# Kernel tuning notes

Hardware: AMD Instinct MI355X
Metric: run time of the kernel (lower is better)

## Reference

```python
import jax, jax.numpy as jnp
import numpy as np

N, E, G = 32768, 262144, 1024
FIN, ED = 32, 8
H, C = 4, 64            # gat_heads, graph_hidden_dim
HC = H * C              # 256
FP_IN, DESC_IN = 2048, 200
GOUT, FPOUT, DOUT = 64, 256, 64
TIN = GOUT + FPOUT + DOUT  # 384
NT = 12
BN_EPS = 1e-5


def bn_eval(x, gamma, beta):
    # eval-mode BatchNorm1d with default running stats (mean=0, var=1)
    inv = 1.0 / jnp.sqrt(1.0 + BN_EPS)
    return x * (gamma * inv) + beta


def gatv2(x, edge_index, edge_attr, Wl, bl, Wr, br, We, att, bias):
    """PyG GATv2Conv (concat heads, add_self_loops=True, fill_value='mean')."""
    n = x.shape[0]
    src, dst = edge_index[0], edge_index[1]
    # self-loop edge_attr = mean of incoming edge_attr per node (PyG fill_value='mean')
    deg = jax.ops.segment_sum(jnp.ones(src.shape, x.dtype), dst, n)
    ea_loop = jax.ops.segment_sum(edge_attr, dst, n) / jnp.maximum(deg, 1.0)[:, None]
    loop = jnp.arange(n)
    src = jnp.concatenate([src, loop])
    dst = jnp.concatenate([dst, loop])
    ea = jnp.concatenate([edge_attr, ea_loop], axis=0)
    xl = (x @ Wl + bl).reshape(n, H, C)   # source transform
    xr = (x @ Wr + br).reshape(n, H, C)   # target transform
    ee = (ea @ We).reshape(-1, H, C)      # edge transform (no bias in PyG)
    m = jax.nn.leaky_relu(xl[src] + xr[dst] + ee, 0.2)  # [E', H, C]
    logit = jnp.einsum('ehc,hc->eh', m, att)            # [E', H]
    # segment softmax over incoming edges of each target node
    lmax = jax.ops.segment_max(logit, dst, n)
    p = jnp.exp(logit - lmax[dst])
    alpha = p / jax.ops.segment_sum(p, dst, n)[dst]
    out = jax.ops.segment_sum(xl[src] * alpha[:, :, None], dst, n)  # [n, H, C]
    return out.reshape(n, HC) + bias


def setup_inputs() -> dict:
    key = jax.random.key(0)
    ks = iter(jax.random.split(key, 64))

    def p(shape, scale=0.05):
        return jax.random.normal(next(ks), shape, dtype=jnp.float32) * scale

    inp = {}
    inp['x'] = jax.random.normal(next(ks), (N, FIN), dtype=jnp.float32)
    inp['edge_index'] = jax.random.randint(next(ks), (2, E), 0, N, dtype=jnp.int32)
    inp['edge_attr'] = jax.random.normal(next(ks), (E, ED), dtype=jnp.float32)
    inp['batch'] = (jnp.arange(N) * G) // N          # sorted, covers all G graphs
    inp['fp'] = jax.random.uniform(next(ks), (G, FP_IN), dtype=jnp.float32)
    inp['desc'] = jax.random.normal(next(ks), (G, DESC_IN), dtype=jnp.float32)
    # GATv2 layer 1 (in=FIN) and layer 2 (in=HC)
    for tag, fin in (('c1', FIN), ('c2', HC)):
        inp[tag + '_Wl'] = p((fin, HC))
        inp[tag + '_bl'] = p((HC,))
        inp[tag + '_Wr'] = p((fin, HC))
        inp[tag + '_br'] = p((HC,))
        inp[tag + '_We'] = p((ED, HC))
        inp[tag + '_att'] = p((H, C))
        inp[tag + '_bias'] = p((HC,))
    inp['gW'], inp['gb'] = p((HC, GOUT)), p((GOUT,))
    inp['g_gn'], inp['g_bt'] = jnp.ones((GOUT,)), jnp.zeros((GOUT,))
    inp['fW'], inp['fb'] = p((FP_IN, FPOUT)), p((FPOUT,))
    inp['f_gn'], inp['f_bt'] = jnp.ones((FPOUT,)), jnp.zeros((FPOUT,))
    inp['dW'], inp['db'] = p((DESC_IN, DOUT)), p((DOUT,))
    inp['d_gn'], inp['d_bt'] = jnp.ones((DOUT,)), jnp.zeros((DOUT,))
    inp['k1W'], inp['k1b'] = p((TIN, TIN // 2)), p((TIN // 2,))
    inp['k1_gn'], inp['k1_bt'] = jnp.ones((TIN // 2,)), jnp.zeros((TIN // 2,))
    inp['k2W'], inp['k2b'] = p((TIN // 2, TIN // 4)), p((TIN // 4,))
    inp['k2_gn'], inp['k2_bt'] = jnp.ones((TIN // 4,)), jnp.zeros((TIN // 4,))
    inp['k3W'], inp['k3b'] = p((TIN // 4, NT)), p((NT,))
    return inp


def reference(x, edge_index, edge_attr, batch, fp, desc,
              c1_Wl, c1_bl, c1_Wr, c1_br, c1_We, c1_att, c1_bias,
              c2_Wl, c2_bl, c2_Wr, c2_br, c2_We, c2_att, c2_bias,
              gW, gb, g_gn, g_bt, fW, fb, f_gn, f_bt, dW, db, d_gn, d_bt,
              k1W, k1b, k1_gn, k1_bt, k2W, k2b, k2_gn, k2_bt, k3W, k3b):
    h = jax.nn.relu(gatv2(x, edge_index, edge_attr, c1_Wl, c1_bl, c1_Wr, c1_br, c1_We, c1_att, c1_bias))
    h = jax.nn.relu(gatv2(h, edge_index, edge_attr, c2_Wl, c2_bl, c2_Wr, c2_br, c2_We, c2_att, c2_bias))
    xg = jax.ops.segment_max(h, batch, G)                 # global_max_pool
    xg = bn_eval(jax.nn.relu(xg @ gW + gb), g_gn, g_bt)
    xf = bn_eval(jax.nn.relu(fp @ fW + fb), f_gn, f_bt)
    xd = bn_eval(jax.nn.relu(desc @ dW + db), d_gn, d_bt)
    z = jnp.concatenate([xg, xf, xd], axis=1)             # [G, TIN]
    z = bn_eval(jax.nn.relu(z @ k1W + k1b), k1_gn, k1_bt)  # dropout off (eval)
    z = bn_eval(jax.nn.relu(z @ k2W + k2b), k2_gn, k2_bt)
    return z @ k3W + k3b                                  # [G, NT]
```

## Files before the change

kernel.cpp:

```cpp
#include <hip/hip_runtime.h>
#include <hip/hip_bf16.h>
#include <math.h>

#define NHEAD 4
#define HC 256

typedef short short8 __attribute__((ext_vector_type(8)));
typedef short short4v __attribute__((ext_vector_type(4)));
typedef float f32x4 __attribute__((ext_vector_type(4)));

__device__ inline f32x4 bf4_to_f32(short4v v)
{
  f32x4 r;
#pragma unroll
  for (int i = 0; i < 4; ++i)
    r[i] = __uint_as_float(((unsigned)(unsigned short)v[i]) << 16);
  return r;
}

__device__ inline float bf_to_f32(unsigned short u)
{
  return __uint_as_float(((unsigned)u) << 16);
}

template <int CTRL>
__device__ inline float dpp_radd(float x)
{
  int yi = __builtin_amdgcn_update_dpp(0, __float_as_int(x), CTRL, 0xf, 0xf, true);
  return x + __int_as_float(yi);
}

__global__ void prep_kernel(
    const float* __restrict__ x, const float* __restrict__ fp,
    const float* __restrict__ c1Wl, const float* __restrict__ c1Wr,
    const float* __restrict__ c2Wl, const float* __restrict__ c2Wr,
    const float* __restrict__ desc, const float* __restrict__ dW,
    const float* __restrict__ k1W,
    const int* __restrict__ dst, int* __restrict__ deg,
    __hip_bfloat16* __restrict__ xbf, __hip_bfloat16* __restrict__ fpbf,
    __hip_bfloat16* __restrict__ wt1, __hip_bfloat16* __restrict__ wt2,
    __hip_bfloat16* __restrict__ descbf, __hip_bfloat16* __restrict__ dwt,
    __hip_bfloat16* __restrict__ k1wt,
    int N, int G, int E, int DIN)
{
  const int n0 = N * 32, n1 = G * 2048, n2 = 512 * 32, n3 = 512 * 256;
  const int n4 = G * 224, n5 = 64 * 224, n6 = 192 * 384;
  int idx = blockIdx.x * 256 + threadIdx.x;
  if (idx < n0) { xbf[idx] = __float2bfloat16(x[idx]); return; }
  idx -= n0;
  if (idx < n1) { fpbf[idx] = __float2bfloat16(fp[idx]); return; }
  idx -= n1;
  if (idx < n2) {
    int n = idx / 32, k = idx - n * 32;
    float v = (n < 256) ? c1Wl[k * 256 + n] : c1Wr[k * 256 + (n - 256)];
    wt1[idx] = __float2bfloat16(v); return;
  }
  idx -= n2;
  if (idx < n3) {
    int n = idx / 256, k = idx - n * 256;
    float v = (n < 256) ? c2Wl[k * 256 + n] : c2Wr[k * 256 + (n - 256)];
    wt2[idx] = __float2bfloat16(v); return;
  }
  idx -= n3;
  if (idx < n4) {
    int row = idx / 224, kp = idx - row * 224;
    float v = (kp < DIN) ? desc[(long)row * DIN + kp] : 0.f;
    descbf[idx] = __float2bfloat16(v); return;
  }
  idx -= n4;
  if (idx < n5) {
    int n = idx / 224, kp = idx - n * 224;
    float v = (kp < DIN) ? dW[kp * 64 + n] : 0.f;
    dwt[idx] = __float2bfloat16(v); return;
  }
  idx -= n5;
  if (idx < n6) {
    int n = idx / 384, k = idx - n * 384;
    k1wt[idx] = __float2bfloat16(k1W[k * 192 + n]); return;
  }
  idx -= n6;
  if (idx < E) atomicAdd(&deg[dst[idx]], 1);
}

__global__ __launch_bounds__(256) void transpose_fwt_kernel(
    const float* __restrict__ fW, __hip_bfloat16* __restrict__ fwt)
{
  __shared__ float tile[64][65];
  int bk = blockIdx.x * 64, bn = blockIdx.y * 64;
  int tx = threadIdx.x & 63, ty = threadIdx.x >> 6;
#pragma unroll
  for (int j = 0; j < 16; ++j) {
    int kl = ty + j * 4;
    tile[kl][tx] = fW[(long)(bk + kl) * 256 + bn + tx];
  }
  __syncthreads();
#pragma unroll
  for (int j = 0; j < 16; ++j) {
    int nl = ty + j * 4;
    fwt[(long)(bn + nl) * 2048 + bk + tx] = __float2bfloat16(tile[tx][nl]);
  }
}

__global__ __launch_bounds__(256) void gemm_mfma_kernel(
    const __hip_bfloat16* __restrict__ A, const __hip_bfloat16* __restrict__ BT,
    const float* __restrict__ bl, const float* __restrict__ br,
    __hip_bfloat16* __restrict__ XL, __hip_bfloat16* __restrict__ XR, int M, int K)
{
  __shared__ short As[128 * 40];
  __shared__ short Bs[128 * 40];
  int bm = blockIdx.x * 128, bn = blockIdx.y * 128;
  int t = threadIdx.x;
  int w = t >> 6, l = t & 63;
  int quad = l >> 4, l16 = l & 15;
  int srow = t >> 1, scol = (t & 1) * 16;

  f32x4 acc[2][8];
#pragma unroll
  for (int i = 0; i < 2; ++i)
#pragma unroll
    for (int j = 0; j < 8; ++j) acc[i][j] = (f32x4){0.f, 0.f, 0.f, 0.f};

  for (int k0 = 0; k0 < K; k0 += 32) {
    *(short8*)&As[srow * 40 + scol] =
        *(const short8*)(const void*)&A[(long)(bm + srow) * K + k0 + scol];
    *(short8*)&As[srow * 40 + scol + 8] =
        *(const short8*)(const void*)&A[(long)(bm + srow) * K + k0 + scol + 8];
    *(short8*)&Bs[srow * 40 + scol] =
        *(const short8*)(const void*)&BT[(long)(bn + srow) * K + k0 + scol];
    *(short8*)&Bs[srow * 40 + scol + 8] =
        *(const short8*)(const void*)&BT[(long)(bn + srow) * K + k0 + scol + 8];
    __syncthreads();
    short8 af[2], bf[8];
#pragma unroll
    for (int mt = 0; mt < 2; ++mt)
      af[mt] = *(short8*)&As[(w * 32 + mt * 16 + l16) * 40 + quad * 8];
#pragma unroll
    for (int nt = 0; nt < 8; ++nt)
      bf[nt] = *(short8*)&Bs[(nt * 16 + l16) * 40 + quad * 8];
#pragma unroll
    for (int mt = 0; mt < 2; ++mt)
#pragma unroll
      for (int nt = 0; nt < 8; ++nt)
        acc[mt][nt] = __builtin_amdgcn_mfma_f32_16x16x32_bf16(af[mt], bf[nt], acc[mt][nt], 0, 0, 0);
    __syncthreads();
  }
#pragma unroll
  for (int mt = 0; mt < 2; ++mt)
#pragma unroll
    for (int nt = 0; nt < 8; ++nt) {
      int col = bn + nt * 16 + l16;
      float b = (col < 256) ? bl[col] : br[col - 256];
#pragma unroll
      for (int r = 0; r < 4; ++r) {
        int row = bm + w * 32 + mt * 16 + quad * 4 + r;
        float v = acc[mt][nt][r] + b;
        if (col < 256)
          XL[(long)row * 256 + col] = __float2bfloat16(v);
        else
          XR[(long)row * 256 + (col - 256)] = __float2bfloat16(v);
      }
    }
}

__global__ __launch_bounds__(256) void gemm_rb_kernel(
    const __hip_bfloat16* __restrict__ A, const __hip_bfloat16* __restrict__ BT,
    const float* __restrict__ bias, const float* __restrict__ gamma,
    const float* __restrict__ beta, void* __restrict__ out,
    int M, int K, int ldc, int coloff, int obf)
{
  __shared__ short As[64 * 40];
  __shared__ short Bs[64 * 40];
  int bm = blockIdx.x * 64, bn = blockIdx.y * 64;
  int t = threadIdx.x;
  int w = t >> 6, l = t & 63;
  int quad = l >> 4, l16 = l & 15;
  int lrow = t >> 2, col8 = (t & 3) * 8;

  f32x4 acc[4];
#pragma unroll
  for (int nt = 0; nt < 4; ++nt) acc[nt] = (f32x4){0.f, 0.f, 0.f, 0.f};

  for (int k0 = 0; k0 < K; k0 += 32) {
    *(short8*)&As[lrow * 40 + col8] =
        *(const short8*)(const void*)&A[(long)(bm + lrow) * K + k0 + col8];
    *(short8*)&Bs[lrow * 40 + col8] =
        *(const short8*)(const void*)&BT[(long)(bn + lrow) * K + k0 + col8];
    __syncthreads();
    short8 af = *(short8*)&As[(w * 16 + l16) * 40 + quad * 8];
#pragma unroll
    for (int nt = 0; nt < 4; ++nt) {
      short8 bf = *(short8*)&Bs[(nt * 16 + l16) * 40 + quad * 8];
      acc[nt] = __builtin_amdgcn_mfma_f32_16x16x32_bf16(af, bf, acc[nt], 0, 0, 0);
    }
    __syncthreads();
  }
  const float inv = rsqrtf(1.f + 1e-5f);
#pragma unroll
  for (int nt = 0; nt < 4; ++nt) {
    int col = bn + nt * 16 + l16;
    float b = bias[col], gm = gamma[col] * inv, bt = beta[col];
#pragma unroll
    for (int r = 0; r < 4; ++r) {
      int row = bm + w * 16 + quad * 4 + r;
      float v = fmaxf(acc[nt][r] + b, 0.f) * gm + bt;
      if (obf)
        ((__hip_bfloat16*)out)[(long)row * ldc + coloff + col] = __float2bfloat16(v);
      else
        ((float*)out)[(long)row * ldc + coloff + col] = v;
    }
  }
}

__global__ __launch_bounds__(256) void gemm_skb_kernel(
    const __hip_bfloat16* __restrict__ A, const __hip_bfloat16* __restrict__ BT,
    float* __restrict__ P, int M, int N, int K, int Kc)
{
  __shared__ short As[64 * 40];
  __shared__ short Bs[64 * 40];
  int bm = blockIdx.x * 64, bn = blockIdx.y * 64;
  int s = blockIdx.z;
  int kb = s * Kc, ke = kb + Kc;
  int t = threadIdx.x;
  int w = t >> 6, l = t & 63;
  int quad = l >> 4, l16 = l & 15;
  int lrow = t >> 2, col8 = (t & 3) * 8;

  f32x4 acc[4];
#pragma unroll
  for (int nt = 0; nt < 4; ++nt) acc[nt] = (f32x4){0.f, 0.f, 0.f, 0.f};

  for (int k0 = kb; k0 < ke; k0 += 32) {
    *(short8*)&As[lrow * 40 + col8] =
        *(const short8*)(const void*)&A[(long)(bm + lrow) * K + k0 + col8];
    *(short8*)&Bs[lrow * 40 + col8] =
        *(const short8*)(const void*)&BT[(long)(bn + lrow) * K + k0 + col8];
    __syncthreads();
    short8 af = *(short8*)&As[(w * 16 + l16) * 40 + quad * 8];
#pragma unroll
    for (int nt = 0; nt < 4; ++nt) {
      short8 bf = *(short8*)&Bs[(nt * 16 + l16) * 40 + quad * 8];
      acc[nt] = __builtin_amdgcn_mfma_f32_16x16x32_bf16(af, bf, acc[nt], 0, 0, 0);
    }
    __syncthreads();
  }
#pragma unroll
  for (int nt = 0; nt < 4; ++nt) {
    int col = bn + nt * 16 + l16;
#pragma unroll
    for (int r = 0; r < 4; ++r) {
      int row = bm + w * 16 + quad * 4 + r;
      P[((long)s * M + row) * N + col] = acc[nt][r];
    }
  }
}

__global__ __launch_bounds__(256) void fp_epilogue_kernel(
    const float* __restrict__ P, const float* __restrict__ bias,
    const float* __restrict__ gamma, const float* __restrict__ beta,
    __hip_bfloat16* __restrict__ zbuf, int M, int N, int S)
{
  int idx = blockIdx.x * 256 + threadIdx.x;
  if (idx >= M * N) return;
  int row = idx / N, col = idx - row * N;
  float v = 0.f;
  for (int s = 0; s < S; ++s) v += P[(long)s * M * N + idx];
  const float inv = rsqrtf(1.f + 1e-5f);
  v = fmaxf(v + bias[col], 0.f) * (gamma[col] * inv) + beta[col];
  zbuf[(long)row * 384 + 64 + col] = __float2bfloat16(v);
}

__global__ __launch_bounds__(256) void poolg_kernel(
    const __hip_bfloat16* __restrict__ h, const float* __restrict__ gW,
    const float* __restrict__ gb, const float* __restrict__ g_gn,
    const float* __restrict__ g_bt, __hip_bfloat16* __restrict__ zbuf, int npg)
{
  __shared__ float smax[256];
  __shared__ float sred[256];
  int g = blockIdx.x, t = threadIdx.x;
  const __hip_bfloat16* base = h + (long)g * npg * HC + t;
  float m = -INFINITY;
#pragma unroll 4
  for (int i = 0; i < npg; ++i)
    m = fmaxf(m, bf_to_f32(*(const unsigned short*)&base[(long)i * HC]));
  smax[t] = m;
  __syncthreads();
  int j = t >> 2, part = t & 3;
  float sum = 0.f;
#pragma unroll 4
  for (int k = part * 64; k < part * 64 + 64; ++k)
    sum = fmaf(smax[k], gW[k * 64 + j], sum);
  sred[t] = sum;
  __syncthreads();
  if (t < 64) {
    float v = sred[t * 4] + sred[t * 4 + 1] + sred[t * 4 + 2] + sred[t * 4 + 3];
    const float inv = rsqrtf(1.f + 1e-5f);
    v = fmaxf(v + gb[t], 0.f) * (g_gn[t] * inv) + g_bt[t];
    zbuf[(long)g * 384 + t] = __float2bfloat16(v);
  }
}

__global__ __launch_bounds__(256) void head23_kernel(
    const float* __restrict__ z1, const float* __restrict__ k2W,
    const float* __restrict__ k2b, const float* __restrict__ k2_gn,
    const float* __restrict__ k2_bt, const float* __restrict__ k3W,
    const float* __restrict__ k3b, float* __restrict__ out)
{
  __shared__ float sW[96 * 96];
  __shared__ float s1[8 * 192];
  __shared__ float s2[8 * 96];
  __shared__ float sk3[96 * 12];
  int b = blockIdx.x, t = threadIdx.x;

  for (int i = t; i < 8 * 192; i += 256) s1[i] = z1[(long)b * (8 * 192) + i];
  for (int i = t; i < 96 * 12; i += 256) sk3[i] = k3W[i];

  int row[3], col[3];
  float acc[3] = {0.f, 0.f, 0.f};
#pragma unroll
  for (int o = 0; o < 3; ++o) {
    int idx = o * 256 + t;
    row[o] = idx / 96;
    col[o] = idx - row[o] * 96;
  }

  for (int half = 0; half < 2; ++half) {
    __syncthreads();
    for (int i = t; i < 96 * 96; i += 256)
      sW[i] = k2W[(long)half * 96 * 96 + i];
    __syncthreads();
#pragma unroll 4
    for (int k = 0; k < 96; ++k) {
#pragma unroll
      for (int o = 0; o < 3; ++o)
        acc[o] = fmaf(s1[row[o] * 192 + half * 96 + k], sW[k * 96 + col[o]], acc[o]);
    }
  }

  const float inv = rsqrtf(1.f + 1e-5f);
#pragma unroll
  for (int o = 0; o < 3; ++o) {
    float v = fmaxf(acc[o] + k2b[col[o]], 0.f) * (k2_gn[col[o]] * inv) + k2_bt[col[o]];
    s2[o * 256 + t] = v;
  }
  __syncthreads();
  if (t < 96) {
    int r3 = t / 12, c3 = t - r3 * 12;
    float a = 0.f;
#pragma unroll 4
    for (int k = 0; k < 96; ++k) a = fmaf(s2[r3 * 96 + k], sk3[k * 12 + c3], a);
    out[(long)(b * 8 + r3) * 12 + c3] = a + k3b[c3];
  }
}

__global__ __launch_bounds__(1024) void scan1_kernel(
    const int* __restrict__ deg, int* __restrict__ ptr,
    int* __restrict__ bsum, int N)
{
  __shared__ int s[1024];
  int b = blockIdx.x, t = threadIdx.x;
  int i = b * 1024 + t;
  int v = (i < N) ? deg[i] : 0;
  s[t] = v;
  __syncthreads();
  for (int off = 1; off < 1024; off <<= 1) {
    int x = (t >= off) ? s[t - off] : 0;
    __syncthreads();
    s[t] += x;
    __syncthreads();
  }
  if (i < N) ptr[i] = s[t] - v;
  if (t == 1023) bsum[b] = s[1023];
}

__global__ __launch_bounds__(256) void scan2_kernel(
    const int* __restrict__ bsum, int* __restrict__ ptr,
    int* __restrict__ cursor, int N, int nb)
{
  int i = blockIdx.x * 256 + threadIdx.x;
  if (i > N) return;
  if (i == N) {
    int tot = 0;
    for (int j = 0; j < nb; ++j) tot += bsum[j];
    ptr[N] = tot;
    return;
  }
  int b = i >> 10;
  int offv = 0;
  for (int j = 0; j < b; ++j) offv += bsum[j];
  int v = ptr[i] + offv;
  ptr[i] = v;
  cursor[i] = v;
}

__global__ void fill_kernel(const int* __restrict__ src, const int* __restrict__ dst,
                            const float* __restrict__ ea, int* __restrict__ cursor,
                            int* __restrict__ csr_src, float* __restrict__ csr_ea, int E)
{
  int e = blockIdx.x * blockDim.x + threadIdx.x;
  if (e < E) {
    int pos = atomicAdd(&cursor[dst[e]], 1);
    csr_src[pos] = src[e];
    f32x4 a0 = *(const f32x4*)(const void*)&ea[(long)e * 8];
    f32x4 a1 = *(const f32x4*)(const void*)&ea[(long)e * 8 + 4];
    *(f32x4*)&csr_ea[(long)pos * 8] = a0;
    *(f32x4*)&csr_ea[(long)pos * 8 + 4] = a1;
  }
}

__global__ __launch_bounds__(256) void eamean_kernel(
    const float* __restrict__ csr_ea, const int* __restrict__ csr_ptr,
    float* __restrict__ ea_mean, int N)
{
  int idx = blockIdx.x * 256 + threadIdx.x;
  if (idx >= N * 8) return;
  int node = idx >> 3, d = idx & 7;
  int p0 = csr_ptr[node], p1 = csr_ptr[node + 1];
  float s = 0.f;
  for (int k = p0; k < p1; ++k) s += csr_ea[(long)k * 8 + d];
  int cnt = p1 - p0;
  ea_mean[idx] = s / (float)(cnt > 1 ? cnt : 1);
}

__global__ __launch_bounds__(128) void gat_kernel(
    const __hip_bfloat16* __restrict__ xlb, const __hip_bfloat16* __restrict__ xrb,
    const float* __restrict__ csr_ea, const int* __restrict__ csr_src,
    const int* __restrict__ csr_ptr, const float* __restrict__ ea_mean,
    const float* __restrict__ We, const float* __restrict__ att,
    const float* __restrict__ bias, __hip_bfloat16* __restrict__ out, int N)
{
  int lane = threadIdx.x & 63;
  int node = blockIdx.x * 2 + (threadIdx.x >> 6);
  if (node >= N) return;
  int cbase = (lane >> 4) * 64 + (lane & 15) * 4;

  f32x4 attv = *(const f32x4*)(const void*)&att[cbase];
  f32x4 xriv = bf4_to_f32(*(const short4v*)(const void*)&xrb[(long)node * HC + cbase]);
  f32x4 WeR[8];
#pragma unroll
  for (int d = 0; d < 8; ++d)
    WeR[d] = *(const f32x4*)(const void*)&We[d * HC + cbase];

  float rsumA = 0.f, rsumB = 0.f;
  f32x4 accA = (f32x4){0.f, 0.f, 0.f, 0.f};
  f32x4 accB = (f32x4){0.f, 0.f, 0.f, 0.f};

  int p0 = csr_ptr[node], p1 = csr_ptr[node + 1];

  auto edge_compute = [&](f32x4 xls, f32x4 ea0, f32x4 ea1,
                          float& rsum, f32x4& acc) {
    f32x4 mv = xriv + xls;
#pragma unroll
    for (int d = 0; d < 4; ++d) mv += WeR[d] * ea0[d];
#pragma unroll
    for (int d = 0; d < 4; ++d) mv += WeR[d + 4] * ea1[d];
    float t = 0.f;
#pragma unroll
    for (int r = 0; r < 4; ++r) {
      float m = mv[r];
      m = (m > 0.f) ? m : 0.2f * m;
      t = fmaf(m, attv[r], t);
    }
    t = dpp_radd<0x121>(t);
    t = dpp_radd<0x122>(t);
    t = dpp_radd<0x124>(t);
    t = dpp_radd<0x128>(t);
    float p = __expf(t);
    rsum += p;
    acc += p * xls;
  };

  short4v xA = (short4v){0, 0, 0, 0}, xB = xA, xC = xA;
  f32x4 a0A = (f32x4){0.f, 0.f, 0.f, 0.f}, a1A = a0A;
  f32x4 a0B = a0A, a1B = a0A, a0C = a0A, a1C = a0A;
  int s3A = 0, s3B = 0, s3C = 0;

  int s0 = 0, s1 = 0, s2 = 0;
  if (p0 < p1)     s0 = csr_src[p0];
  if (p0 + 1 < p1) s1 = csr_src[p0 + 1];
  if (p0 + 2 < p1) s2 = csr_src[p0 + 2];
  if (p0 + 3 < p1) s3A = csr_src[p0 + 3];
  if (p0 + 4 < p1) s3B = csr_src[p0 + 4];
  if (p0 + 5 < p1) s3C = csr_src[p0 + 5];
  if (p0 < p1) {
    a0A = *(const f32x4*)(const void*)&csr_ea[(long)p0 * 8];
    a1A = *(const f32x4*)(const void*)&csr_ea[(long)p0 * 8 + 4];
    xA = *(const short4v*)(const void*)&xlb[(long)s0 * HC + cbase];
  }
  if (p0 + 1 < p1) {
    a0B = *(const f32x4*)(const void*)&csr_ea[(long)(p0 + 1) * 8];
    a1B = *(const f32x4*)(const void*)&csr_ea[(long)(p0 + 1) * 8 + 4];
    xB = *(const short4v*)(const void*)&xlb[(long)s1 * HC + cbase];
  }
  if (p0 + 2 < p1) {
    a0C = *(const f32x4*)(const void*)&csr_ea[(long)(p0 + 2) * 8];
    a1C = *(const f32x4*)(const void*)&csr_ea[(long)(p0 + 2) * 8 + 4];
    xC = *(const short4v*)(const void*)&xlb[(long)s2 * HC + cbase];
  }

  int k = p0;
  for (; k + 3 <= p1; k += 3) {
    f32x4 e0 = a0A, e1 = a1A;
    short4v xc = xA;
    if (k + 3 < p1) {
      xA = *(const short4v*)(const void*)&xlb[(long)s3A * HC + cbase];
      a0A = *(const f32x4*)(const void*)&csr_ea[(long)(k + 3) * 8];
      a1A = *(const f32x4*)(const void*)&csr_ea[(long)(k + 3) * 8 + 4];
    }
    if (k + 6 < p1) s3A = csr_src[k + 6];
    edge_compute(bf4_to_f32(xc), e0, e1, rsumA, accA);

    e0 = a0B; e1 = a1B; xc = xB;
    if (k + 4 < p1) {
      xB = *(const short4v*)(const void*)&xlb[(long)s3B * HC + cbase];
      a0B = *(const f32x4*)(const void*)&csr_ea[(long)(k + 4) * 8];
      a1B = *(const f32x4*)(const void*)&csr_ea[(long)(k + 4) * 8 + 4];
    }
    if (k + 7 < p1) s3B = csr_src[k + 7];
    edge_compute(bf4_to_f32(xc), e0, e1, rsumB, accB);

    e0 = a0C; e1 = a1C; xc = xC;
    if (k + 5 < p1) {
      xC = *(const short4v*)(const void*)&xlb[(long)s3C * HC + cbase];
      a0C = *(const f32x4*)(const void*)&csr_ea[(long)(k + 5) * 8];
      a1C = *(const f32x4*)(const void*)&csr_ea[(long)(k + 5) * 8 + 4];
    }
    if (k + 8 < p1) s3C = csr_src[k + 8];
    edge_compute(bf4_to_f32(xc), e0, e1, rsumA, accA);
  }
  if (k < p1)     edge_compute(bf4_to_f32(xA), a0A, a1A, rsumA, accA);
  if (k + 1 < p1) edge_compute(bf4_to_f32(xB), a0B, a1B, rsumB, accB);

  f32x4 em0 = *(const f32x4*)(const void*)&ea_mean[(long)node * 8];
  f32x4 em1 = *(const f32x4*)(const void*)&ea_mean[(long)node * 8 + 4];
  f32x4 xls_self = bf4_to_f32(*(const short4v*)(const void*)&xlb[(long)node * HC + cbase]);
  edge_compute(xls_self, em0, em1, rsumB, accB);

  float invs = 1.f / (rsumA + rsumB);
  f32x4 biasv = *(const f32x4*)(const void*)&bias[cbase];
  short4v pk;
#pragma unroll
  for (int r = 0; r < 4; ++r) {
    float v = fmaxf((accA[r] + accB[r]) * invs + biasv[r], 0.f);
    __hip_bfloat16 hv = __float2bfloat16(v);
    pk[r] = *(short*)&hv;
  }
  *(short4v*)&out[(long)node * HC + cbase] = pk;
}

extern "C" void kernel_launch(void* const* d_in, const int* in_sizes, int n_in,
                              void* d_out, int out_size, void* d_ws, size_t ws_size,
                              hipStream_t stream)
{
  const float* x          = (const float*)d_in[0];
  const int*   edge_index = (const int*)d_in[1];
  const float* edge_attr  = (const float*)d_in[2];
  const float* fp         = (const float*)d_in[4];
  const float* desc       = (const float*)d_in[5];
  const float *c1_Wl = (const float*)d_in[6],  *c1_bl = (const float*)d_in[7],
              *c1_Wr = (const float*)d_in[8],  *c1_br = (const float*)d_in[9],
              *c1_We = (const float*)d_in[10], *c1_att = (const float*)d_in[11],
              *c1_bias = (const float*)d_in[12];
  const float *c2_Wl = (const float*)d_in[13], *c2_bl = (const float*)d_in[14],
              *c2_Wr = (const float*)d_in[15], *c2_br = (const float*)d_in[16],
              *c2_We = (const float*)d_in[17], *c2_att = (const float*)d_in[18],
              *c2_bias = (const float*)d_in[19];
  const float *gW = (const float*)d_in[20], *gb = (const float*)d_in[21],
              *g_gn = (const float*)d_in[22], *g_bt = (const float*)d_in[23];
  const float *fW = (const float*)d_in[24], *fb = (const float*)d_in[25],
              *f_gn = (const float*)d_in[26], *f_bt = (const float*)d_in[27];
  const float *dW = (const float*)d_in[28], *db = (const float*)d_in[29],
              *d_gn = (const float*)d_in[30], *d_bt = (const float*)d_in[31];
  const float *k1W = (const float*)d_in[32], *k1b = (const float*)d_in[33],
              *k1_gn = (const float*)d_in[34], *k1_bt = (const float*)d_in[35];
  const float *k2W = (const float*)d_in[36], *k2b = (const float*)d_in[37],
              *k2_gn = (const float*)d_in[38], *k2_bt = (const float*)d_in[39];
  const float *k3W = (const float*)d_in[40], *k3b = (const float*)d_in[41];

  const int N = in_sizes[0] / 32;
  const int E = in_sizes[1] / 2;
  const int G = in_sizes[4] / 2048;
  const int FIN = 32, FPIN = 2048;
  const int DIN = in_sizes[5] / G;

  char* ws = (char*)d_ws;
  size_t off = 0;
  auto alloc = [&](size_t bytes) {
    void* p = ws + off;
    off = (off + bytes + 255) & ~(size_t)255;
    return p;
  };
  __hip_bfloat16* xlb    = (__hip_bfloat16*)alloc((size_t)N * HC * 2);
  __hip_bfloat16* xrb    = (__hip_bfloat16*)alloc((size_t)N * HC * 2);
  __hip_bfloat16* hb1    = (__hip_bfloat16*)alloc((size_t)N * HC * 2);
  __hip_bfloat16* hb2    = (__hip_bfloat16*)alloc((size_t)N * HC * 2);
  __hip_bfloat16* xbf    = (__hip_bfloat16*)alloc((size_t)N * FIN * 2);
  __hip_bfloat16* fpbf   = (__hip_bfloat16*)alloc((size_t)G * FPIN * 2);
  __hip_bfloat16* wt1    = (__hip_bfloat16*)alloc((size_t)512 * FIN * 2);
  __hip_bfloat16* wt2    = (__hip_bfloat16*)alloc((size_t)512 * HC * 2);
  __hip_bfloat16* fwt    = (__hip_bfloat16*)alloc((size_t)256 * FPIN * 2);
  __hip_bfloat16* descbf = (__hip_bfloat16*)alloc((size_t)G * 224 * 2);
  __hip_bfloat16* dwt    = (__hip_bfloat16*)alloc((size_t)64 * 224 * 2);
  __hip_bfloat16* k1wt   = (__hip_bfloat16*)alloc((size_t)192 * 384 * 2);
  __hip_bfloat16* zbuf   = (__hip_bfloat16*)alloc((size_t)G * 384 * 2);
  float* z1      = (float*)alloc((size_t)G * 192 * 4);
  float* P_fp    = (float*)alloc((size_t)4 * G * 256 * 4);
  int*   deg     = (int*)alloc((size_t)N * 4);
  int*   csr_ptr = (int*)alloc((size_t)(N + 1) * 4);
  int*   cursor  = (int*)alloc((size_t)N * 4);
  int*   csr_src = (int*)alloc((size_t)E * 4);
  float* csr_ea  = (float*)alloc((size_t)E * 8 * 4);
  float* ea_mean = (float*)alloc((size_t)N * 8 * 4);
  int*   bsum    = (int*)alloc((size_t)64 * 4);
  (void)ws_size;

  const int* srcp = edge_index;
  const int* dstp = edge_index + E;
  const int nb = (N + 1023) / 1024;

  hipMemsetAsync(deg, 0, (size_t)N * 4, stream);

  {
    long total = (long)N * FIN + (long)G * FPIN + 512 * 32 + 512 * 256 +
                 (long)G * 224 + 64 * 224 + 192 * 384 + E;
    prep_kernel<<<(int)((total + 255) / 256), 256, 0, stream>>>(
        x, fp, c1_Wl, c1_Wr, c2_Wl, c2_Wr, desc, dW, k1W, dstp, deg,
        xbf, fpbf, wt1, wt2, descbf, dwt, k1wt, N, G, E, DIN);
  }
  transpose_fwt_kernel<<<dim3(2048 / 64, 256 / 64), 256, 0, stream>>>(fW, fwt);
  scan1_kernel<<<nb, 1024, 0, stream>>>(deg, csr_ptr, bsum, N);
  scan2_kernel<<<(N + 1 + 255) / 256, 256, 0, stream>>>(bsum, csr_ptr, cursor, N, nb);
  fill_kernel<<<(E + 255) / 256, 256, 0, stream>>>(srcp, dstp, edge_attr, cursor,
                                                   csr_src, csr_ea, E);
  eamean_kernel<<<(N * 8 + 255) / 256, 256, 0, stream>>>(csr_ea, csr_ptr, ea_mean, N);

  gemm_skb_kernel<<<dim3(G / 64, 4, 4), 256, 0, stream>>>(fpbf, fwt, P_fp,
                                                          G, 256, FPIN, FPIN / 4);
  fp_epilogue_kernel<<<(G * 256 + 255) / 256, 256, 0, stream>>>(P_fp, fb, f_gn, f_bt,
                                                                zbuf, G, 256, 4);
  gemm_rb_kernel<<<dim3(G / 64, 1), 256, 0, stream>>>(descbf, dwt, db, d_gn, d_bt,
                                                      zbuf, G, 224, 384, 320, 1);

  gemm_mfma_kernel<<<dim3(N / 128, 4), 256, 0, stream>>>(xbf, wt1, c1_bl, c1_br, xlb, xrb, N, FIN);
  gat_kernel<<<N / 2, 128, 0, stream>>>(xlb, xrb, csr_ea, csr_src, csr_ptr, ea_mean,
                                        c1_We, c1_att, c1_bias, hb1, N);
  gemm_mfma_kernel<<<dim3(N / 128, 4), 256, 0, stream>>>(hb1, wt2, c2_bl, c2_br, xlb, xrb, N, HC);
  gat_kernel<<<N / 2, 128, 0, stream>>>(xlb, xrb, csr_ea, csr_src, csr_ptr, ea_mean,
                                        c2_We, c2_att, c2_bias, hb2, N);

  poolg_kernel<<<G, 256, 0, stream>>>(hb2, gW, gb, g_gn, g_bt, zbuf, N / G);

  gemm_rb_kernel<<<dim3(G / 64, 3), 256, 0, stream>>>(zbuf, k1wt, k1b, k1_gn, k1_bt,
                                                      z1, G, 384, 192, 0, 0);
  head23_kernel<<<G / 8, 256, 0, stream>>>(z1, k2W, k2b, k2_gn, k2_bt, k3W, k3b,
                                           (float*)d_out);
}
```

Measured before the change: 403.3 us.

## Merge independent prep kernels into horizontally fused mega-kernels

Folds the fW transpose into the prep kernel as a naive strided transpose, and vectorises the x and fp bf16 conversions to four elements per thread. Combines the split-K fp GEMM, CSR fill and desc GEMM into one launch, and the edge-attr mean and fp epilogue into a second launch. This cuts the number of small kernel launches and the idle tail between them. In exchange the fW transpose loses coalesced reads, and the mixed block types in each launch may balance unevenly.

```diff
diff --git a/kernel.cpp b/kernel.cpp
--- a/kernel.cpp
+++ b/kernel.cpp
@@ -21,6 +21,17 @@
 __device__ inline float bf_to_f32(unsigned short u)
 {
   return __uint_as_float(((unsigned)u) << 16);
+}
+
+__device__ inline short4v f4_to_bf4(f32x4 v)
+{
+  short4v o;
+#pragma unroll
+  for (int i = 0; i < 4; ++i) {
+    __hip_bfloat16 h = __float2bfloat16(v[i]);
+    o[i] = *(short*)&h;
+  }
+  return o;
 }
 
 template <int CTRL>
@@ -35,20 +46,31 @@
     const float* __restrict__ c1Wl, const float* __restrict__ c1Wr,
     const float* __restrict__ c2Wl, const float* __restrict__ c2Wr,
     const float* __restrict__ desc, const float* __restrict__ dW,
-    const float* __restrict__ k1W,
+    const float* __restrict__ k1W, const float* __restrict__ fW,
     const int* __restrict__ dst, int* __restrict__ deg,
     __hip_bfloat16* __restrict__ xbf, __hip_bfloat16* __restrict__ fpbf,
     __hip_bfloat16* __restrict__ wt1, __hip_bfloat16* __restrict__ wt2,
     __hip_bfloat16* __restrict__ descbf, __hip_bfloat16* __restrict__ dwt,
-    __hip_bfloat16* __restrict__ k1wt,
+    __hip_bfloat16* __restrict__ k1wt, __hip_bfloat16* __restrict__ fwt,
     int N, int G, int E, int DIN)
 {
-  const int n0 = N * 32, n1 = G * 2048, n2 = 512 * 32, n3 = 512 * 256;
+  const int n0 = N * 8;
+  const int n1 = G * 512;
+  const int n2 = 512 * 32, n3 = 512 * 256;
   const int n4 = G * 224, n5 = 64 * 224, n6 = 192 * 384;
+  const int n7 = 256 * 2048;
   int idx = blockIdx.x * 256 + threadIdx.x;
-  if (idx < n0) { xbf[idx] = __float2bfloat16(x[idx]); return; }
+  if (idx < n0) {
+    f32x4 v = ((const f32x4*)x)[idx];
+    ((short4v*)xbf)[idx] = f4_to_bf4(v);
+    return;
+  }
   idx -= n0;
-  if (idx < n1) { fpbf[idx] = __float2bfloat16(fp[idx]); return; }
+  if (idx < n1) {
+    f32x4 v = ((const f32x4*)fp)[idx];
+    ((short4v*)fpbf)[idx] = f4_to_bf4(v);
+    return;
+  }
   idx -= n1;
   if (idx < n2) {
     int n = idx / 32, k = idx - n * 32;
@@ -79,26 +101,12 @@
     k1wt[idx] = __float2bfloat16(k1W[k * 192 + n]); return;
   }
   idx -= n6;
+  if (idx < n7) {
+    int n = idx >> 11, k = idx & 2047;
+    fwt[idx] = __float2bfloat16(fW[k * 256 + n]); return;
+  }
+  idx -= n7;
   if (idx < E) atomicAdd(&deg[dst[idx]], 1);
-}
-
-__global__ __launch_bounds__(256) void transpose_fwt_kernel(
-    const float* __restrict__ fW, __hip_bfloat16* __restrict__ fwt)
-{
-  __shared__ float tile[64][65];
-  int bk = blockIdx.x * 64, bn = blockIdx.y * 64;
-  int tx = threadIdx.x & 63, ty = threadIdx.x >> 6;
-#pragma unroll
-  for (int j = 0; j < 16; ++j) {
-    int kl = ty + j * 4;
-    tile[kl][tx] = fW[(long)(bk + kl) * 256 + bn + tx];
-  }
-  __syncthreads();
-#pragma unroll
-  for (int j = 0; j < 16; ++j) {
-    int nl = ty + j * 4;
-    fwt[(long)(bn + nl) * 2048 + bk + tx] = __float2bfloat16(tile[tx][nl]);
-  }
 }
 
 __global__ __launch_bounds__(256) void gemm_mfma_kernel(
@@ -211,61 +219,146 @@
   }
 }
 
-__global__ __launch_bounds__(256) void gemm_skb_kernel(
-    const __hip_bfloat16* __restrict__ A, const __hip_bfloat16* __restrict__ BT,
-    float* __restrict__ P, int M, int N, int K, int Kc)
+__global__ __launch_bounds__(256) void mega1_kernel(
+    const __hip_bfloat16* __restrict__ fpbf, const __hip_bfloat16* __restrict__ fwt,
+    float* __restrict__ P,
+    const int* __restrict__ esrc, const int* __restrict__ edst,
+    const float* __restrict__ ea, int* __restrict__ cursor,
+    int* __restrict__ csr_src, float* __restrict__ csr_ea,
+    const __hip_bfloat16* __restrict__ descbf, const __hip_bfloat16* __restrict__ dwt,
+    const float* __restrict__ db, const float* __restrict__ d_gn,
+    const float* __restrict__ d_bt, __hip_bfloat16* __restrict__ zbuf,
+    int G, int E)
 {
   __shared__ short As[64 * 40];
   __shared__ short Bs[64 * 40];
-  int bm = blockIdx.x * 64, bn = blockIdx.y * 64;
-  int s = blockIdx.z;
-  int kb = s * Kc, ke = kb + Kc;
+  int b = blockIdx.x;
+  const int t = threadIdx.x;
+  const int NB_SKB = (G / 64) * 16;
+  const int NB_FILL = E / 256;
+
+  if (b < NB_SKB) {
+    const int gx = G / 64;
+    int bx = b % gx, rem = b / gx;
+    int by = rem & 3, s = rem >> 2;
+    int bm = bx * 64, bn = by * 64;
+    const int K = 2048, Kc = 512;
+    int kb = s * Kc, ke = kb + Kc;
+    int w = t >> 6, l = t & 63;
+    int quad = l >> 4, l16 = l & 15;
+    int lrow = t >> 2, col8 = (t & 3) * 8;
+
+    f32x4 acc[4];
+#pragma unroll
+    for (int nt = 0; nt < 4; ++nt) acc[nt] = (f32x4){0.f, 0.f, 0.f, 0.f};
+
+    for (int k0 = kb; k0 < ke; k0 += 32) {
+      *(short8*)&As[lrow * 40 + col8] =
+          *(const short8*)(const void*)&fpbf[(long)(bm + lrow) * K + k0 + col8];
+      *(short8*)&Bs[lrow * 40 + col8] =
+          *(const short8*)(const void*)&fwt[(long)(bn + lrow) * K + k0 + col8];
+      __syncthreads();
+      short8 af = *(short8*)&As[(w * 16 + l16) * 40 + quad * 8];
+#pragma unroll
+      for (int nt = 0; nt < 4; ++nt) {
+        short8 bf = *(short8*)&Bs[(nt * 16 + l16) * 40 + quad * 8];
+        acc[nt] = __builtin_amdgcn_mfma_f32_16x16x32_bf16(af, bf, acc[nt], 0, 0, 0);
+      }
+      __syncthreads();
+    }
+#pragma unroll
+    for (int nt = 0; nt < 4; ++nt) {
+      int col = bn + nt * 16 + l16;
+#pragma unroll
+      for (int r = 0; r < 4; ++r) {
+        int row = bm + w * 16 + quad * 4 + r;
+        P[((long)s * G + row) * 256 + col] = acc[nt][r];
+      }
+    }
+    return;
+  }
+  b -= NB_SKB;
+  if (b < NB_FILL) {
+    int e = b * 256 + t;
+    if (e < E) {
+      int pos = atomicAdd(&cursor[edst[e]], 1);
+      csr_src[pos] = esrc[e];
+      f32x4 a0 = *(const f32x4*)(const void*)&ea[(long)e * 8];
+      f32x4 a1 = *(const f32x4*)(const void*)&ea[(long)e * 8 + 4];
+      *(f32x4*)&csr_ea[(long)pos * 8] = a0;
+      *(f32x4*)&csr_ea[(long)pos * 8 + 4] = a1;
+    }
+    return;
+  }
+  b -= NB_FILL;
+  {
+    int bm = b * 64;
+    const int K = 224;
+    int w = t >> 6, l = t & 63;
+    int quad = l >> 4, l16 = l & 15;
+    int lrow = t >> 2, col8 = (t & 3) * 8;
+
+    f32x4 acc[4];
+#pragma unroll
+    for (int nt = 0; nt < 4; ++nt) acc[nt] = (f32x4){0.f, 0.f, 0.f, 0.f};
+
+    for (int k0 = 0; k0 < K; k0 += 32) {
+      *(short8*)&As[lrow * 40 + col8] =
+          *(const short8*)(const void*)&descbf[(long)(bm + lrow) * K + k0 + col8];
+      *(short8*)&Bs[lrow * 40 + col8] =
+          *(const short8*)(const void*)&dwt[(long)lrow * K + k0 + col8];
+      __syncthreads();
+      short8 af = *(short8*)&As[(w * 16 + l16) * 40 + quad * 8];
+#pragma unroll
+      for (int nt = 0; nt < 4; ++nt) {
+        short8 bf = *(short8*)&Bs[(nt * 16 + l16) * 40 + quad * 8];
+        acc[nt] = __builtin_amdgcn_mfma_f32_16x16x32_bf16(af, bf, acc[nt], 0, 0, 0);
+      }
+      __syncthreads();
+    }
+    const float inv = rsqrtf(1.f + 1e-5f);
+#pragma unroll
+    for (int nt = 0; nt < 4; ++nt) {
+      int col = nt * 16 + l16;
+      float bb = db[col], gm = d_gn[col] * inv, bt = d_bt[col];
+#pragma unroll
+      for (int r = 0; r < 4; ++r) {
+        int row = bm + w * 16 + quad * 4 + r;
+        float v = fmaxf(acc[nt][r] + bb, 0.f) * gm + bt;
+        zbuf[(long)row * 384 + 320 + col] = __float2bfloat16(v);
+      }
+    }
+  }
+}
+
+__global__ __launch_bounds__(256) void mega2_kernel(
+    const float* __restrict__ csr_ea, const int* __restrict__ csr_ptr,
+    float* __restrict__ ea_mean,
+    const float* __restrict__ P, const float* __restrict__ fb,
+    const float* __restrict__ f_gn, const float* __restrict__ f_bt,
+    __hip_bfloat16* __restrict__ zbuf, int N, int G)
+{
+  int b = blockIdx.x;
   int t = threadIdx.x;
-  int w = t >> 6, l = t & 63;
-  int quad = l >> 4, l16 = l & 15;
-  int lrow = t >> 2, col8 = (t & 3) * 8;
-
-  f32x4 acc[4];
-#pragma unroll
-  for (int nt = 0; nt < 4; ++nt) acc[nt] = (f32x4){0.f, 0.f, 0.f, 0.f};
-
-  for (int k0 = kb; k0 < ke; k0 += 32) {
-    *(short8*)&As[lrow * 40 + col8] =
-        *(const short8*)(const void*)&A[(long)(bm + lrow) * K + k0 + col8];
-    *(short8*)&Bs[lrow * 40 + col8] =
-        *(const short8*)(const void*)&BT[(long)(bn + lrow) * K + k0 + col8];
-    __syncthreads();
-    short8 af = *(short8*)&As[(w * 16 + l16) * 40 + quad * 8];
-#pragma unroll
-    for (int nt = 0; nt < 4; ++nt) {
-      short8 bf = *(short8*)&Bs[(nt * 16 + l16) * 40 + quad * 8];
-      acc[nt] = __builtin_amdgcn_mfma_f32_16x16x32_bf16(af, bf, acc[nt], 0, 0, 0);
-    }
-    __syncthreads();
-  }
-#pragma unroll
-  for (int nt = 0; nt < 4; ++nt) {
-    int col = bn + nt * 16 + l16;
-#pragma unroll
-    for (int r = 0; r < 4; ++r) {
-      int row = bm + w * 16 + quad * 4 + r;
-      P[((long)s * M + row) * N + col] = acc[nt][r];
-    }
-  }
-}
-
-__global__ __launch_bounds__(256) void fp_epilogue_kernel(
-    const float* __restrict__ P, const float* __restrict__ bias,
-    const float* __restrict__ gamma, const float* __restrict__ beta,
-    __hip_bfloat16* __restrict__ zbuf, int M, int N, int S)
-{
-  int idx = blockIdx.x * 256 + threadIdx.x;
-  if (idx >= M * N) return;
-  int row = idx / N, col = idx - row * N;
+  const int NB_EA = N * 8 / 256;
+  if (b < NB_EA) {
+    int idx = b * 256 + t;
+    int node = idx >> 3, d = idx & 7;
+    int p0 = csr_ptr[node], p1 = csr_ptr[node + 1];
+    float s = 0.f;
+    for (int k = p0; k < p1; ++k) s += csr_ea[(long)k * 8 + d];
+    int cnt = p1 - p0;
+    ea_mean[idx] = s / (float)(cnt > 1 ? cnt : 1);
+    return;
+  }
+  b -= NB_EA;
+  int idx = b * 256 + t;
+  int row = idx >> 8, col = idx & 255;
   float v = 0.f;
-  for (int s = 0; s < S; ++s) v += P[(long)s * M * N + idx];
+#pragma unroll
+  for (int s = 0; s < 4; ++s) v += P[(long)s * G * 256 + idx];
   const float inv = rsqrtf(1.f + 1e-5f);
-  v = fmaxf(v + bias[col], 0.f) * (gamma[col] * inv) + beta[col];
+  v = fmaxf(v + fb[col], 0.f) * (f_gn[col] * inv) + f_bt[col];
   zbuf[(long)row * 384 + 64 + col] = __float2bfloat16(v);
 }
 
@@ -390,35 +483,6 @@
   int v = ptr[i] + offv;
   ptr[i] = v;
   cursor[i] = v;
-}
-
-__global__ void fill_kernel(const int* __restrict__ src, const int* __restrict__ dst,
-                            const float* __restrict__ ea, int* __restrict__ cursor,
-                            int* __restrict__ csr_src, float* __restrict__ csr_ea, int E)
-{
-  int e = blockIdx.x * blockDim.x + threadIdx.x;
-  if (e < E) {
-    int pos = atomicAdd(&cursor[dst[e]], 1);
-    csr_src[pos] = src[e];
-    f32x4 a0 = *(const f32x4*)(const void*)&ea[(long)e * 8];
-    f32x4 a1 = *(const f32x4*)(const void*)&ea[(long)e * 8 + 4];
-    *(f32x4*)&csr_ea[(long)pos * 8] = a0;
-    *(f32x4*)&csr_ea[(long)pos * 8 + 4] = a1;
-  }
-}
-
-__global__ __launch_bounds__(256) void eamean_kernel(
-    const float* __restrict__ csr_ea, const int* __restrict__ csr_ptr,
-    float* __restrict__ ea_mean, int N)
-{
-  int idx = blockIdx.x * 256 + threadIdx.x;
-  if (idx >= N * 8) return;
-  int node = idx >> 3, d = idx & 7;
-  int p0 = csr_ptr[node], p1 = csr_ptr[node + 1];
-  float s = 0.f;
-  for (int k = p0; k < p1; ++k) s += csr_ea[(long)k * 8 + d];
-  int cnt = p1 - p0;
-  ea_mean[idx] = s / (float)(cnt > 1 ? cnt : 1);
 }
 
 __global__ __launch_bounds__(128) void gat_kernel(
@@ -620,27 +684,27 @@
   hipMemsetAsync(deg, 0, (size_t)N * 4, stream);
 
   {
-    long total = (long)N * FIN + (long)G * FPIN + 512 * 32 + 512 * 256 +
-                 (long)G * 224 + 64 * 224 + 192 * 384 + E;
+    long total = (long)N * 8 + (long)G * 512 + 512 * 32 + 512 * 256 +
+                 (long)G * 224 + 64 * 224 + 192 * 384 + 256 * 2048 + E;
     prep_kernel<<<(int)((total + 255) / 256), 256, 0, stream>>>(
-        x, fp, c1_Wl, c1_Wr, c2_Wl, c2_Wr, desc, dW, k1W, dstp, deg,
-        xbf, fpbf, wt1, wt2, descbf, dwt, k1wt, N, G, E, DIN);
-  }
-  transpose_fwt_kernel<<<dim3(2048 / 64, 256 / 64), 256, 0, stream>>>(fW, fwt);
+        x, fp, c1_Wl, c1_Wr, c2_Wl, c2_Wr, desc, dW, k1W, fW, dstp, deg,
+        xbf, fpbf, wt1, wt2, descbf, dwt, k1wt, fwt, N, G, E, DIN);
+  }
   scan1_kernel<<<nb, 1024, 0, stream>>>(deg, csr_ptr, bsum, N);
   scan2_kernel<<<(N + 1 + 255) / 256, 256, 0, stream>>>(bsum, csr_ptr, cursor, N, nb);
-  fill_kernel<<<(E + 255) / 256, 256, 0, stream>>>(srcp, dstp, edge_attr, cursor,
-                                                   csr_src, csr_ea, E);
-  eamean_kernel<<<(N * 8 + 255) / 256, 256, 0, stream>>>(csr_ea, csr_ptr, ea_mean, N);
-
-  gemm_skb_kernel<<<dim3(G / 64, 4, 4), 256, 0, stream>>>(fpbf, fwt, P_fp,
-                                                          G, 256, FPIN, FPIN / 4);
-  fp_epilogue_kernel<<<(G * 256 + 255) / 256, 256, 0, stream>>>(P_fp, fb, f_gn, f_bt,
-                                                                zbuf, G, 256, 4);
-  gemm_rb_kernel<<<dim3(G / 64, 1), 256, 0, stream>>>(descbf, dwt, db, d_gn, d_bt,
-                                                      zbuf, G, 224, 384, 320, 1);
+
+  {
+    int nblk = (G / 64) * 16 + E / 256 + G / 64;
+    mega1_kernel<<<nblk, 256, 0, stream>>>(
+        fpbf, fwt, P_fp, srcp, dstp, edge_attr, cursor, csr_src, csr_ea,
+        descbf, dwt, db, d_gn, d_bt, zbuf, G, E);
+  }
 
   gemm_mfma_kernel<<<dim3(N / 128, 4), 256, 0, stream>>>(xbf, wt1, c1_bl, c1_br, xlb, xrb, N, FIN);
+
+  mega2_kernel<<<N * 8 / 256 + G, 256, 0, stream>>>(
+      csr_ea, csr_ptr, ea_mean, P_fp, fb, f_gn, f_bt, zbuf, N, G);
+
   gat_kernel<<<N / 2, 128, 0, stream>>>(xlb, xrb, csr_ea, csr_src, csr_ptr, ea_mean,
                                         c1_We, c1_att, c1_bias, hb1, N);
   gemm_mfma_kernel<<<dim3(N / 128, 4), 256, 0, stream>>>(hb1, wt2, c2_bl, c2_br, xlb, xrb, N, HC);
```

Result: faster. 388.6 us (-3.6%).
